# Optimization experiments

Measured on AMD Instinct MI355X. Metric: run time of the kernel, lower is better.

Reference implementation:

```python
import jax, jax.numpy as jnp
from jax import lax
import numpy as np

B, N, NPOINT, NSAMPLE, C = 4, 16384, 1024, 32, 64
RADIUS2 = 0.1 ** 2
BIG = 1e10


def fps(xyz, npoint):
    """Furthest point sampling. xyz: (B,N,3) -> idx (B,npoint) int32."""
    b, n, _ = xyz.shape

    def step(carry, _):
        dists, farthest = carry                      # (B,N), (B,)
        centroid = jnp.take_along_axis(xyz, farthest[:, None, None], axis=1)  # (B,1,3)
        d = jnp.sum((xyz - centroid) ** 2, axis=-1)  # (B,N)
        dists = jnp.minimum(dists, d)
        nxt = jnp.argmax(dists, axis=-1).astype(jnp.int32)
        return (dists, nxt), farthest

    init = (jnp.full((b, n), BIG, xyz.dtype), jnp.zeros((b,), jnp.int32))
    _, idx = lax.scan(step, init, None, length=npoint)
    return jnp.transpose(idx)  # (B,npoint)


def ball_query(xyz, new_xyz, r2, nsample):
    """First nsample neighbor indices within radius; pad with first hit."""
    n = xyz.shape[1]
    d2 = jnp.sum((new_xyz[:, :, None, :] - xyz[:, None, :, :]) ** 2, axis=-1)  # (B,NP,N)
    within = d2 < r2
    score = jnp.where(within, jnp.arange(n, dtype=jnp.int32), n)  # index if inside ball else N
    neg_vals, _ = lax.top_k(-score, nsample)   # smallest scores (earliest indices)
    idx = -neg_vals                            # (B,NP,nsample), ascending
    first = idx[..., 0:1]
    return jnp.where(idx < n, idx, first)


def setup_inputs() -> dict:
    key = jax.random.key(0)
    ks = jax.random.split(key, 8)
    xyz = jax.random.uniform(ks[0], (B, N, 3), dtype=jnp.float32)
    features = jax.random.normal(ks[1], (B, N, C), dtype=jnp.float32)
    cin = 3 + C
    def init_w(k, o, i):
        return jax.random.normal(k, (o, i), dtype=jnp.float32) * (1.0 / np.sqrt(i))
    return {
        "xyz": xyz,
        "features": features,
        "w1": init_w(ks[2], 64, cin), "b1": jnp.zeros((64,), jnp.float32),
        "w2": init_w(ks[3], 64, 64),  "b2": jnp.zeros((64,), jnp.float32),
        "w3": init_w(ks[4], 128, 64), "b3": jnp.zeros((128,), jnp.float32),
    }


def reference(xyz, features, w1, b1, w2, b2, w3, b3):
    # --- FPS sampling of centers ---
    fidx = fps(xyz, NPOINT)                                        # (B,NP)
    new_xyz = jnp.take_along_axis(xyz, fidx[..., None], axis=1)    # (B,NP,3)
    # --- ball-query grouping ---
    nidx = ball_query(xyz, new_xyz, RADIUS2, NSAMPLE)              # (B,NP,NS)
    flat = nidx.reshape(B, NPOINT * NSAMPLE)
    g_xyz = jnp.take_along_axis(xyz, flat[..., None], axis=1).reshape(B, NPOINT, NSAMPLE, 3)
    g_xyz = g_xyz - new_xyz[:, :, None, :]                         # center-relative coords
    g_feat = jnp.take_along_axis(features, flat[..., None], axis=1).reshape(B, NPOINT, NSAMPLE, C)
    h = jnp.concatenate([g_xyz, g_feat], axis=-1)                  # (B,NP,NS,3+C)
    # --- shared 1x1-conv MLP + ReLU ---
    h = jax.nn.relu(jnp.einsum('bpsc,oc->bpso', h, w1) + b1)
    h = jax.nn.relu(jnp.einsum('bpsc,oc->bpso', h, w2) + b2)
    h = jax.nn.relu(jnp.einsum('bpsc,oc->bpso', h, w3) + b3)       # (B,NP,NS,128)
    # --- max pool over neighbors ---
    new_features = jnp.transpose(jnp.max(h, axis=2), (0, 2, 1))    # (B,128,NP)
    return new_xyz, new_features
```

## Files before the change

kernel.cpp:

```cpp
#include <hip/hip_runtime.h>
#include <stdint.h>

#define BB 4
#define NN 16384
#define NPOINT 1024
#define NSAMPLE 32
#define CC 64
#define RADIUS2 0.00999999977648258209228515625f
#define BIGF 1.0e10f

#define FT 1024
#define NPAIR 8

typedef float f32x2 __attribute__((ext_vector_type(2)));

__global__ __launch_bounds__(256) void repack_w1(const float* __restrict__ w1,
                                                 float* __restrict__ w1p) {
    int t = threadIdx.x;
    for (int i = t; i < 64 * 68; i += 256) {
        int o = i / 68, c = i % 68;
        w1p[i] = (c < 67) ? w1[o * 67 + c] : 0.0f;
    }
}

template <int CTRL>
__device__ __forceinline__ void amax_step(float& v, int& i) {
    int nv = __builtin_amdgcn_update_dpp(__float_as_int(v), __float_as_int(v),
                                         CTRL, 0xf, 0xf, false);
    int ni = __builtin_amdgcn_update_dpp(i, i, CTRL, 0xf, 0xf, false);
    float fv = __int_as_float(nv);
    if (fv > v || (fv == v && ni < i)) { v = fv; i = ni; }
}
__device__ __forceinline__ void wave_amax(float& v, int& i) {
    amax_step<0x111>(v, i);
    amax_step<0x112>(v, i);
    amax_step<0x114>(v, i);
    amax_step<0x118>(v, i);
    amax_step<0x142>(v, i);
    amax_step<0x143>(v, i);
}

__global__ __launch_bounds__(FT)
void fps_kernel(const float* xyz, float* new_xyz) {
    const int b = blockIdx.x;
    const int t = threadIdx.x;
    const int lane = t & 63;
    const int w = t >> 6;

    __shared__ float sx[NN];
    __shared__ float sy[NN];
    __shared__ float st[3 * NPOINT];
    __shared__ float2 svi[2][16];

    const float* xb = xyz + (size_t)b * NN * 3;

    f32x2 pz[NPAIR];
    f32x2 dd[NPAIR];

#pragma unroll
    for (int k = 0; k < NPAIR; ++k) {
        const float* p = xb + (size_t)6 * (k * FT + t);
        f32x2 a = *(const f32x2*)(p + 0);
        f32x2 bq = *(const f32x2*)(p + 2);
        f32x2 c = *(const f32x2*)(p + 4);
        int g = 2 * (k * FT + t);
        f32x2 vx; vx.x = a.x; vx.y = bq.y;
        f32x2 vy; vy.x = a.y; vy.y = c.x;
        *(f32x2*)&sx[g] = vx;
        *(f32x2*)&sy[g] = vy;
        pz[k].x = bq.x; pz[k].y = c.y;
        dd[k].x = BIGF; dd[k].y = BIGF;
    }
#pragma unroll
    for (int k = 0; k < NPAIR; ++k) asm("" : "+v"(pz[k]));

    float cx = xb[0], cy = xb[1], cz = xb[2];
    __syncthreads();

    for (int i = 0; i < NPOINT; ++i) {
        if (t == 0) {
            st[3 * i + 0] = cx; st[3 * i + 1] = cy; st[3 * i + 2] = cz;
        }
        if (i == NPOINT - 1) break;

        f32x2 vx[NPAIR], vy[NPAIR];
#pragma unroll
        for (int k = 0; k < NPAIR; ++k) {
            vx[k] = *(const f32x2*)&sx[2 * (k * FT + t)];
            vy[k] = *(const f32x2*)&sy[2 * (k * FT + t)];
        }

        float bv = -1.0f;
        int bj = 0;
#pragma unroll
        for (int k = 0; k < NPAIR; ++k) {
            float dx0 = __fsub_rn(vx[k].x, cx);
            float dy0 = __fsub_rn(vy[k].x, cy);
            float dz0 = __fsub_rn(pz[k].x, cz);
            float d0 = __fadd_rn(__fadd_rn(__fmul_rn(dx0, dx0),
                                           __fmul_rn(dy0, dy0)),
                                 __fmul_rn(dz0, dz0));
            float dx1 = __fsub_rn(vx[k].y, cx);
            float dy1 = __fsub_rn(vy[k].y, cy);
            float dz1 = __fsub_rn(pz[k].y, cz);
            float d1 = __fadd_rn(__fadd_rn(__fmul_rn(dx1, dx1),
                                           __fmul_rn(dy1, dy1)),
                                 __fmul_rn(dz1, dz1));
            dd[k].x = fminf(dd[k].x, d0);
            dd[k].y = fminf(dd[k].y, d1);
            if (dd[k].x > bv) { bv = dd[k].x; bj = 2 * k; }
            if (dd[k].y > bv) { bv = dd[k].y; bj = 2 * k + 1; }
        }
        int bi = (bj >> 1) * (2 * FT) + 2 * t + (bj & 1);

        wave_amax(bv, bi);
        if (lane == 63) svi[i & 1][w] = make_float2(bv, __int_as_float(bi));
        __syncthreads();

        float2 s = svi[i & 1][lane & 15];
        float v2 = s.x;
        int i2 = __float_as_int(s.y);
        amax_step<0x111>(v2, i2);
        amax_step<0x112>(v2, i2);
        amax_step<0x114>(v2, i2);
        amax_step<0x118>(v2, i2);
        int ixs = __builtin_amdgcn_readlane(i2, 63);

        cx = sx[ixs];
        cy = sy[ixs];
        cz = xb[ixs * 3 + 2];
    }

    __syncthreads();
    float* ob = new_xyz + (size_t)b * NPOINT * 3;
#pragma unroll
    for (int j = 0; j < 3; ++j) ob[j * FT + t] = st[j * FT + t];
}

__global__ __launch_bounds__(256) void ballquery_kernel(const float* __restrict__ xyz,
                                                        const float* __restrict__ new_xyz,
                                                        int* __restrict__ nidx) {
    const int t = threadIdx.x;
    const int lane = t & 63;
    const int w = t >> 6;
    const int cid = blockIdx.x * 4 + w;
    const int b = cid >> 10;

    __shared__ int list[4][NSAMPLE];

    const float* xb = xyz + (size_t)b * NN * 3;
    const float* c = new_xyz + (size_t)cid * 3;
    float cx = c[0], cy = c[1], cz = c[2];

    int cnt = 0;
    for (int base = 0; base < NN && cnt < NSAMPLE; base += 64) {
        int j = base + lane;
        float dx = __fsub_rn(xb[j * 3 + 0], cx);
        float dy = __fsub_rn(xb[j * 3 + 1], cy);
        float dz = __fsub_rn(xb[j * 3 + 2], cz);
        float d2 = __fadd_rn(__fadd_rn(__fmul_rn(dx, dx), __fmul_rn(dy, dy)),
                             __fmul_rn(dz, dz));
        bool hit = d2 < RADIUS2;
        unsigned long long m = __ballot(hit);
        int pre = __popcll(m & ((1ull << lane) - 1ull));
        if (hit) {
            int pos = cnt + pre;
            if (pos < NSAMPLE) list[w][pos] = j;
        }
        cnt += __popcll(m);
    }
    __syncthreads();
    if (lane < NSAMPLE) {
        int first = list[w][0];
        int v = (lane < cnt) ? list[w][lane] : first;
        nidx[(size_t)cid * NSAMPLE + lane] = v;
    }
}

__global__ __launch_bounds__(256, 2) void mlp_kernel(
    const float* __restrict__ xyz, const float* __restrict__ features,
    const float* __restrict__ new_xyz, const int* __restrict__ nidx,
    const float* __restrict__ w1p, const float* __restrict__ b1,
    const float* __restrict__ w2, const float* __restrict__ b2,
    const float* __restrict__ w3, const float* __restrict__ b3,
    float* __restrict__ out) {
    const int gid = blockIdx.x * 256 + threadIdx.x;
    const int s = gid & 31;
    const int pg = gid >> 5;
    const int b = pg >> 10;
    const int p = pg & 1023;

    const int idx = nidx[gid];
    const float* nc = new_xyz + (size_t)pg * 3;
    const float* pt = xyz + ((size_t)b * NN + idx) * 3;
    float gx = pt[0] - nc[0], gy = pt[1] - nc[1], gz = pt[2] - nc[2];

    float fin[64];
    const float4* fp = (const float4*)(features + ((size_t)b * NN + idx) * CC);
#pragma unroll
    for (int j = 0; j < 16; ++j) {
        float4 q = fp[j];
        fin[4 * j] = q.x; fin[4 * j + 1] = q.y;
        fin[4 * j + 2] = q.z; fin[4 * j + 3] = q.w;
    }

    float h1[64];
#pragma unroll
    for (int o = 0; o < 64; ++o) {
        const float4* wr = (const float4*)(w1p + o * 68);
        float acc = b1[o];
        float4 q0 = wr[0];
        acc = fmaf(q0.x, gx, acc);
        acc = fmaf(q0.y, gy, acc);
        acc = fmaf(q0.z, gz, acc);
        acc = fmaf(q0.w, fin[0], acc);
#pragma unroll
        for (int j = 1; j < 17; ++j) {
            float4 q = wr[j];
            int c0 = 4 * j - 3;
            acc = fmaf(q.x, fin[c0], acc);
            acc = fmaf(q.y, fin[c0 + 1], acc);
            acc = fmaf(q.z, fin[c0 + 2], acc);
            if (c0 + 3 < 64) acc = fmaf(q.w, fin[c0 + 3], acc);
        }
        h1[o] = fmaxf(acc, 0.0f);
    }

    float h2[64];
#pragma unroll
    for (int o = 0; o < 64; ++o) {
        const float4* wr = (const float4*)(w2 + o * 64);
        float acc = b2[o];
#pragma unroll
        for (int j = 0; j < 16; ++j) {
            float4 q = wr[j];
            acc = fmaf(q.x, h1[4 * j], acc);
            acc = fmaf(q.y, h1[4 * j + 1], acc);
            acc = fmaf(q.z, h1[4 * j + 2], acc);
            acc = fmaf(q.w, h1[4 * j + 3], acc);
        }
        h2[o] = fmaxf(acc, 0.0f);
    }

    float* ob = out + (size_t)b * 128 * NPOINT + p;
#pragma unroll
    for (int o = 0; o < 128; ++o) {
        const float4* wr = (const float4*)(w3 + o * 64);
        float acc = b3[o];
#pragma unroll
        for (int j = 0; j < 16; ++j) {
            float4 q = wr[j];
            acc = fmaf(q.x, h2[4 * j], acc);
            acc = fmaf(q.y, h2[4 * j + 1], acc);
            acc = fmaf(q.z, h2[4 * j + 2], acc);
            acc = fmaf(q.w, h2[4 * j + 3], acc);
        }
        float r = fmaxf(acc, 0.0f);
#pragma unroll
        for (int off = 1; off < 32; off <<= 1) {
            float orr = __shfl_xor(r, off);
            r = fmaxf(r, orr);
        }
        if (s == 0) ob[(size_t)o * NPOINT] = r;
    }
}

extern "C" void kernel_launch(void* const* d_in, const int* in_sizes, int n_in,
                              void* d_out, int out_size, void* d_ws, size_t ws_size,
                              hipStream_t stream) {
    const float* xyz = (const float*)d_in[0];
    const float* features = (const float*)d_in[1];
    const float* w1 = (const float*)d_in[2];
    const float* b1 = (const float*)d_in[3];
    const float* w2 = (const float*)d_in[4];
    const float* b2 = (const float*)d_in[5];
    const float* w3 = (const float*)d_in[6];
    const float* b3 = (const float*)d_in[7];

    float* out = (float*)d_out;
    float* new_xyz = out;
    float* new_feat = out + BB * NPOINT * 3;

    int* nidx = (int*)d_ws;
    float* w1p = (float*)((char*)d_ws + (size_t)BB * NPOINT * NSAMPLE * sizeof(int));

    hipLaunchKernelGGL(repack_w1, dim3(1), dim3(256), 0, stream, w1, w1p);
    hipLaunchKernelGGL(fps_kernel, dim3(BB), dim3(FT), 0, stream, xyz, new_xyz);
    hipLaunchKernelGGL(ballquery_kernel, dim3(BB * NPOINT / 4), dim3(256), 0, stream,
                       xyz, new_xyz, nidx);
    hipLaunchKernelGGL(mlp_kernel, dim3(BB * NPOINT * NSAMPLE / 256), dim3(256), 0, stream,
                       xyz, features, new_xyz, nidx, w1p, b1, w2, b2, w3, b3, new_feat);
}
```

Baseline: 2.542 ms.

## Halve FPS block size, hold all coordinates in registers, use packed float2 math

The FPS kernel now runs 512 threads per block, each owning 32 points, and keeps x, y and z in registers instead of re-reading x and y from LDS every iteration. The distance update uses float2 vector ops that can map to packed FP32 instructions. The argmax is split into a branchless max pass followed by an equality scan for the index. The cross-wave reduction shrinks to 8 waves. The aim is to cut LDS traffic and per-iteration latency on the serial 1024-step loop. The cost is much higher register pressure and fewer waves to hide latency.

```diff
diff --git a/kernel.cpp b/kernel.cpp
--- a/kernel.cpp
+++ b/kernel.cpp
@@ -9,8 +9,8 @@
 #define RADIUS2 0.00999999977648258209228515625f
 #define BIGF 1.0e10f
 
-#define FT 1024
-#define NPAIR 8
+#define FT 512
+#define NPAIR 16
 
 typedef float f32x2 __attribute__((ext_vector_type(2)));
 
@@ -40,7 +40,7 @@
     amax_step<0x143>(v, i);
 }
 
-__global__ __launch_bounds__(FT)
+__global__ __launch_bounds__(FT, 2)
 void fps_kernel(const float* xyz, float* new_xyz) {
     const int b = blockIdx.x;
     const int t = threadIdx.x;
@@ -50,12 +50,11 @@
     __shared__ float sx[NN];
     __shared__ float sy[NN];
     __shared__ float st[3 * NPOINT];
-    __shared__ float2 svi[2][16];
+    __shared__ float2 svi[2][8];
 
     const float* xb = xyz + (size_t)b * NN * 3;
 
-    f32x2 pz[NPAIR];
-    f32x2 dd[NPAIR];
+    f32x2 px[NPAIR], py[NPAIR], pz[NPAIR], dd[NPAIR];
 
 #pragma unroll
     for (int k = 0; k < NPAIR; ++k) {
@@ -64,15 +63,15 @@
         f32x2 bq = *(const f32x2*)(p + 2);
         f32x2 c = *(const f32x2*)(p + 4);
         int g = 2 * (k * FT + t);
-        f32x2 vx; vx.x = a.x; vx.y = bq.y;
-        f32x2 vy; vy.x = a.y; vy.y = c.x;
-        *(f32x2*)&sx[g] = vx;
-        *(f32x2*)&sy[g] = vy;
-        pz[k].x = bq.x; pz[k].y = c.y;
+        px[k].x = a.x;  py[k].x = a.y;  pz[k].x = bq.x;
+        px[k].y = bq.y; py[k].y = c.x;  pz[k].y = c.y;
+        *(f32x2*)&sx[g] = px[k];
+        *(f32x2*)&sy[g] = py[k];
         dd[k].x = BIGF; dd[k].y = BIGF;
     }
 #pragma unroll
-    for (int k = 0; k < NPAIR; ++k) asm("" : "+v"(pz[k]));
+    for (int k = 0; k < NPAIR; ++k)
+        asm("" : "+v"(px[k]), "+v"(py[k]), "+v"(pz[k]));
 
     float cx = xb[0], cy = xb[1], cz = xb[2];
     __syncthreads();
@@ -83,33 +82,32 @@
         }
         if (i == NPOINT - 1) break;
 
-        f32x2 vx[NPAIR], vy[NPAIR];
+        f32x2 c2x; c2x.x = cx; c2x.y = cx;
+        f32x2 c2y; c2y.x = cy; c2y.y = cy;
+        f32x2 c2z; c2z.x = cz; c2z.y = cz;
+
+        float mxx = -1.0f, mxy = -1.0f;
 #pragma unroll
         for (int k = 0; k < NPAIR; ++k) {
-            vx[k] = *(const f32x2*)&sx[2 * (k * FT + t)];
-            vy[k] = *(const f32x2*)&sy[2 * (k * FT + t)];
-        }
-
-        float bv = -1.0f;
+            f32x2 dx = px[k] - c2x;
+            f32x2 dy = py[k] - c2y;
+            f32x2 dz = pz[k] - c2z;
+            f32x2 m0 = dx * dx;
+            f32x2 m1 = dy * dy;
+            f32x2 m2 = dz * dz;
+            f32x2 d  = (m0 + m1) + m2;
+            dd[k].x = fminf(dd[k].x, d.x);
+            dd[k].y = fminf(dd[k].y, d.y);
+            mxx = fmaxf(mxx, dd[k].x);
+            mxy = fmaxf(mxy, dd[k].y);
+        }
+        float bv = fmaxf(mxx, mxy);
+
         int bj = 0;
 #pragma unroll
-        for (int k = 0; k < NPAIR; ++k) {
-            float dx0 = __fsub_rn(vx[k].x, cx);
-            float dy0 = __fsub_rn(vy[k].x, cy);
-            float dz0 = __fsub_rn(pz[k].x, cz);
-            float d0 = __fadd_rn(__fadd_rn(__fmul_rn(dx0, dx0),
-                                           __fmul_rn(dy0, dy0)),
-                                 __fmul_rn(dz0, dz0));
-            float dx1 = __fsub_rn(vx[k].y, cx);
-            float dy1 = __fsub_rn(vy[k].y, cy);
-            float dz1 = __fsub_rn(pz[k].y, cz);
-            float d1 = __fadd_rn(__fadd_rn(__fmul_rn(dx1, dx1),
-                                           __fmul_rn(dy1, dy1)),
-                                 __fmul_rn(dz1, dz1));
-            dd[k].x = fminf(dd[k].x, d0);
-            dd[k].y = fminf(dd[k].y, d1);
-            if (dd[k].x > bv) { bv = dd[k].x; bj = 2 * k; }
-            if (dd[k].y > bv) { bv = dd[k].y; bj = 2 * k + 1; }
+        for (int k = NPAIR - 1; k >= 0; --k) {
+            if (dd[k].y == bv) bj = 2 * k + 1;
+            if (dd[k].x == bv) bj = 2 * k;
         }
         int bi = (bj >> 1) * (2 * FT) + 2 * t + (bj & 1);
 
@@ -117,13 +115,12 @@
         if (lane == 63) svi[i & 1][w] = make_float2(bv, __int_as_float(bi));
         __syncthreads();
 
-        float2 s = svi[i & 1][lane & 15];
+        float2 s = svi[i & 1][lane & 7];
         float v2 = s.x;
         int i2 = __float_as_int(s.y);
         amax_step<0x111>(v2, i2);
         amax_step<0x112>(v2, i2);
         amax_step<0x114>(v2, i2);
-        amax_step<0x118>(v2, i2);
         int ixs = __builtin_amdgcn_readlane(i2, 63);
 
         cx = sx[ixs];
@@ -133,8 +130,7 @@
 
     __syncthreads();
     float* ob = new_xyz + (size_t)b * NPOINT * 3;
-#pragma unroll
-    for (int j = 0; j < 3; ++j) ob[j * FT + t] = st[j * FT + t];
+    for (int j = t; j < 3 * NPOINT; j += FT) ob[j] = st[j];
 }
 
 __global__ __launch_bounds__(256) void ballquery_kernel(const float* __restrict__ xyz,
```

Measured after the change: 2.155 ms, median of 2. 1.18x faster.
